# Performance work log

Measured on AMD Instinct MI355X. Metric: run time of the kernel, lower is better.

Reference implementation:

```python
import jax, jax.numpy as jnp
import numpy as np

N_NODES = 1024  # cities (fully connected graph)
N_HID = 128     # config.N: edge-MLP hidden dim (W2: N_HID x 3)
M = 128         # config.M: embedding dim
T = 4           # config.T: message-passing iterations
TAU = 10.0      # config.tau: softmax temperature


def setup_inputs() -> dict:
    key = jax.random.key(0)
    ks = jax.random.split(key, 18)
    u = lambda k, s: jax.random.uniform(k, s, dtype=jnp.float32)
    return dict(
        D=u(ks[0], (N_NODES, N_NODES)),       # pairwise distances graph[v][u]
        dd=u(ks[1], (N_NODES,)),              # graph[depot][v]
        dr=u(ks[2], (N_NODES,)),              # distance_from_robot()
        ddep=u(ks[3], (N_NODES,)),            # distance_from_depot()
        mu0_A1=u(ks[4], (N_NODES, M)),
        mu0_A2=u(ks[5], (N_NODES, M)),
        mu0_B=u(ks[6], (N_NODES, M)),
        W1=u(ks[7], (1, N_HID)),
        W2=u(ks[8], (N_HID, 3)),
        W3_A1=u(ks[9], (M, M + 1)),
        W3_A2=u(ks[10], (M, M + 1)),
        W4_A1=u(ks[11], (M, 1)),
        W4_A2=u(ks[12], (M, 1)),
        W3_B=u(ks[13], (M, M)),
        W4_B=u(ks[14], (M, 2 * M)),
        W5=u(ks[15], (1, M)),
        W6=u(ks[16], (1, M)),
        W7=u(ks[17], (1, M)),
    )


def _edge_scores(D, dd, W1, W2):
    # G[v,u] = W1 @ relu(W2 @ [D[v,u], dd[v], dd[u]])  -> scalar per pair
    h = (D[:, :, None] * W2[:, 0]
         + dd[:, None, None] * W2[:, 1]
         + dd[None, :, None] * W2[:, 2])            # (n, n, N_HID)
    return jnp.maximum(h, 0.0) @ W1[0]              # (n, n)


def _attn(G):
    # p[u,v] = softmax over sources u != v of G[u,v]/tau
    n = G.shape[0]
    Gm = jnp.where(jnp.eye(n, dtype=bool), -jnp.inf, G / TAU)
    return jax.nn.softmax(Gm, axis=0)


def _layer_A(P, wd, mu, Wg, W3, W4, dist):
    # l_v = [ sum_u p_uv * D[u,v] * relu(Wg @ mu_v) ; sum_u p_uv * mu_u ]
    # mu_v <- relu(W3 @ l_v + W4 * dist_v)
    for _ in range(T):
        s = jnp.maximum(mu @ Wg[0], 0.0)                        # (n,)
        l = jnp.concatenate([(wd * s)[:, None], P.T @ mu], 1)   # (n, M+1)
        mu = jnp.maximum(l @ W3.T + dist[:, None] * W4[:, 0][None, :], 0.0)
    return mu


def reference(D, dd, dr, ddep, mu0_A1, mu0_A2, mu0_B,
              W1, W2, W3_A1, W3_A2, W4_A1, W4_A2, W3_B, W4_B, W5, W6, W7):
    # A1 and B use distances / 1000 for edge scores; A2 uses raw distances.
    G_scaled = _edge_scores(D / 1000.0, dd / 1000.0, W1, W2)
    G_raw = _edge_scores(D, dd, W1, W2)
    P1 = _attn(G_scaled)
    P2 = _attn(G_raw)
    wd1 = jnp.sum(P1 * D, axis=0)   # attention-weighted raw edge distance, per v
    wd2 = jnp.sum(P2 * D, axis=0)

    A1 = _layer_A(P1, wd1, mu0_A1, W5, W3_A1, W4_A1, dr)
    A2 = _layer_A(P2, wd2, mu0_A2, W6, W3_A2, W4_A2, ddep)

    bias = jnp.concatenate([A1, A2], axis=1) @ W4_B.T  # (n, M), constant over t
    mu = mu0_B
    for _ in range(T):
        mu = jnp.maximum((P1.T @ mu) @ W3_B.T + bias, 0.0)

    return jnp.maximum(W7 @ jnp.sum(mu, axis=0)[:, None], 0.0)  # (1, 1)
```

## Files before the change

### kernel.cpp

```cpp
#include <hip/hip_runtime.h>
#include <math.h>

#define N 1024
#define M 128

__global__ __launch_bounds__(256) void k_prep(const float* __restrict__ D, float* __restrict__ DT,
    const float* __restrict__ W3A1, const float* __restrict__ W3A2,
    const float* __restrict__ W3B, const float* __restrict__ W4B,
    float* __restrict__ oA1, float* __restrict__ oA2,
    float* __restrict__ oB, float* __restrict__ o4B,
    float* __restrict__ gsum, unsigned int* __restrict__ gcnt) {
  int bx = blockIdx.x, t = threadIdx.x;
  if (bx < 1024) {
    __shared__ float tile[32 * 33];
    int tx = t & 31, ty = t >> 5;
    int bxx = (bx & 31) * 32, by = (bx >> 5) * 32;
#pragma unroll
    for (int i = 0; i < 4; i++)
      tile[(ty + i * 8) * 33 + tx] = D[(size_t)(by + ty + i * 8) * N + bxx + tx];
    __syncthreads();
#pragma unroll
    for (int i = 0; i < 4; i++)
      DT[(size_t)(bxx + ty + i * 8) * N + by + tx] = tile[tx * 33 + ty + i * 8];
  } else if (bx < 1345) {
    int idx = (bx - 1024) * 256 + t;
    const float* in = nullptr; float* op = nullptr; int cols = 0, o = 0;
    if (idx < 16512)      { in = W3A1; op = oA1; cols = 129; o = idx; }
    else if (idx < 33024) { in = W3A2; op = oA2; cols = 129; o = idx - 16512; }
    else if (idx < 49408) { in = W3B;  op = oB;  cols = 128; o = idx - 33024; }
    else if (idx < 82176) { in = W4B;  op = o4B; cols = 256; o = idx - 49408; }
    if (in) { int r = o & 127, c = o >> 7; op[o] = in[r * cols + c]; }
  } else {
    if (t == 0) { *gsum = 0.f; *gcnt = 0u; }
  }
}

__device__ __forceinline__ float blk_max(float v, float* red, int t) {
#pragma unroll
  for (int o = 32; o; o >>= 1) v = fmaxf(v, __shfl_xor(v, o));
  __syncthreads();
  if ((t & 63) == 0) red[t >> 6] = v;
  __syncthreads();
  return fmaxf(fmaxf(red[0], red[1]), fmaxf(red[2], red[3]));
}
__device__ __forceinline__ float blk_sum(float v, float* red, int t) {
#pragma unroll
  for (int o = 32; o; o >>= 1) v += __shfl_xor(v, o);
  __syncthreads();
  if ((t & 63) == 0) red[t >> 6] = v;
  __syncthreads();
  return red[0] + red[1] + red[2] + red[3];
}

__global__ __launch_bounds__(256) void k_edge(const float* __restrict__ DT,
                                              const float* __restrict__ dd,
                                              const float* __restrict__ W1,
                                              const float* __restrict__ W2,
                                              float* __restrict__ PT1, float* __restrict__ PT2,
                                              float* __restrict__ wd1, float* __restrict__ wd2) {
  __shared__ float4 wp[128];
  __shared__ float red[4];
  int t = threadIdx.x, v = blockIdx.x;
  if (t < 128) {
    float4 p;
    p.x = W2[t * 3 + 0]; p.y = W2[t * 3 + 1]; p.z = W2[t * 3 + 2]; p.w = W1[t];
    wp[t] = p;
  }
  __syncthreads();
  float yv = dd[v];
  float x[4], z[4], g[4] = {0.f, 0.f, 0.f, 0.f};
#pragma unroll
  for (int i = 0; i < 4; i++) {
    int u = t + i * 256;
    x[i] = DT[(size_t)v * N + u];
    z[i] = dd[u];
  }
#pragma unroll 2
  for (int k = 0; k < 128; k++) {
    float4 wk = wp[k];
    float cv = yv * wk.z;
#pragma unroll
    for (int i = 0; i < 4; i++) {
      float h = fmaf(x[i], wk.x, fmaf(z[i], wk.y, cv));
      g[i] = fmaf(fmaxf(h, 0.f), wk.w, g[i]);
    }
  }
#pragma unroll
  for (int i = 0; i < 4; i++)
    if (t + i * 256 == v) g[i] = -INFINITY;
  float m = fmaxf(fmaxf(g[0], g[1]), fmaxf(g[2], g[3]));
  m = blk_max(m, red, t);
  float er[4], es[4], sr = 0.f, ss = 0.f;
#pragma unroll
  for (int i = 0; i < 4; i++) {
    er[i] = expf((g[i] - m) * 0.1f);
    es[i] = expf((g[i] - m) * 1e-4f);
    sr += er[i]; ss += es[i];
  }
  sr = blk_sum(sr, red, t);
  ss = blk_sum(ss, red, t);
  float ir = 1.f / sr, is = 1.f / ss;
  float a1 = 0.f, a2 = 0.f;
#pragma unroll
  for (int i = 0; i < 4; i++) {
    int u = t + i * 256;
    float pr = er[i] * ir, ps = es[i] * is;
    PT2[(size_t)v * N + u] = pr;
    PT1[(size_t)v * N + u] = ps;
    a1 += ps * x[i];
    a2 += pr * x[i];
  }
  a1 = blk_sum(a1, red, t);
  a2 = blk_sum(a2, red, t);
  if (t == 0) { wd1[v] = a1; wd2[v] = a2; }
}

__device__ __forceinline__ void gemm4(const float* __restrict__ PT,
                                      const float* __restrict__ cur,
                                      float* __restrict__ As, float* __restrict__ CsP,
                                      int r0, int t) {
#pragma unroll
  for (int i = 0; i < 4; i++) {
    int idx = t + i * 256;
    int row = idx >> 8, c4 = idx & 255;
    ((float4*)As)[row * 256 + c4] = *((const float4*)(PT + (size_t)(r0 + row) * N) + c4);
  }
  __syncthreads();
  const int kc = t >> 5;
  const int cg = t & 31;
  const int u0 = kc * 128;
  float4 acc0 = {0,0,0,0}, acc1 = {0,0,0,0}, acc2 = {0,0,0,0}, acc3 = {0,0,0,0};
  const float* mub = cur + (size_t)u0 * M + cg * 4;
  const float* a0p = As + u0;
  const float* a1p = As + 1024 + u0;
  const float* a2p = As + 2048 + u0;
  const float* a3p = As + 3072 + u0;
#pragma unroll 2
  for (int uu = 0; uu < 128; uu += 4) {
    float4 a0 = *(const float4*)&a0p[uu];
    float4 a1 = *(const float4*)&a1p[uu];
    float4 a2 = *(const float4*)&a2p[uu];
    float4 a3 = *(const float4*)&a3p[uu];
    float4 b0 = *(const float4*)&mub[(size_t)(uu + 0) * M];
    float4 b1 = *(const float4*)&mub[(size_t)(uu + 1) * M];
    float4 b2 = *(const float4*)&mub[(size_t)(uu + 2) * M];
    float4 b3 = *(const float4*)&mub[(size_t)(uu + 3) * M];
#define FMA4(ACC, AV) \
    ACC.x = fmaf(AV.x, b0.x, ACC.x); ACC.y = fmaf(AV.x, b0.y, ACC.y); \
    ACC.z = fmaf(AV.x, b0.z, ACC.z); ACC.w = fmaf(AV.x, b0.w, ACC.w); \
    ACC.x = fmaf(AV.y, b1.x, ACC.x); ACC.y = fmaf(AV.y, b1.y, ACC.y); \
    ACC.z = fmaf(AV.y, b1.z, ACC.z); ACC.w = fmaf(AV.y, b1.w, ACC.w); \
    ACC.x = fmaf(AV.z, b2.x, ACC.x); ACC.y = fmaf(AV.z, b2.y, ACC.y); \
    ACC.z = fmaf(AV.z, b2.z, ACC.z); ACC.w = fmaf(AV.z, b2.w, ACC.w); \
    ACC.x = fmaf(AV.w, b3.x, ACC.x); ACC.y = fmaf(AV.w, b3.y, ACC.y); \
    ACC.z = fmaf(AV.w, b3.z, ACC.z); ACC.w = fmaf(AV.w, b3.w, ACC.w);
    FMA4(acc0, a0) FMA4(acc1, a1) FMA4(acc2, a2) FMA4(acc3, a3)
#undef FMA4
  }
  float* cp = CsP + kc * 512 + cg * 4;
  *(float4*)&cp[0]   = acc0;
  *(float4*)&cp[128] = acc1;
  *(float4*)&cp[256] = acc2;
  *(float4*)&cp[384] = acc3;
  __syncthreads();
#pragma unroll
  for (int i = 0; i < 2; i++) {
    int j = t + i * 256;
    float s = 0.f;
#pragma unroll
    for (int s8 = 0; s8 < 8; s8++) s += CsP[s8 * 512 + j];
    As[j] = s;
  }
}

__global__ __launch_bounds__(256) void k_iterA(
    const float* __restrict__ PT1, const float* __restrict__ PT2,
    const float* __restrict__ cur1, const float* __restrict__ cur2,
    float* __restrict__ nxt1, float* __restrict__ nxt2,
    const float* __restrict__ wd1, const float* __restrict__ wd2,
    const float* __restrict__ dr, const float* __restrict__ ddep,
    const float* __restrict__ W3A1T, const float* __restrict__ W3A2T,
    const float* __restrict__ W4A1, const float* __restrict__ W4A2,
    const float* __restrict__ W5, const float* __restrict__ W6) {
  __shared__ float smem[4096 + 4096 + 4];
  float* As = smem;
  float* CsP = smem + 4096;
  float* swd = smem + 8192;
  int z = blockIdx.z;
  const float* PT = z ? PT2 : PT1;
  const float* cur = z ? cur2 : cur1;
  float* nxt = z ? nxt2 : nxt1;
  const float* wdv = z ? wd2 : wd1;
  const float* dist = z ? ddep : dr;
  const float* W3T = z ? W3A2T : W3A1T;
  const float* W4c = z ? W4A2 : W4A1;
  const float* Wg = z ? W6 : W5;
  int t = threadIdx.x, r0 = blockIdx.x * 4;

  gemm4(PT, cur, As, CsP, r0, t);
  {
    int row = t >> 6, l = t & 63;
    const float* mo = cur + (size_t)(r0 + row) * M;
    float sp = fmaf(mo[l], Wg[l], mo[l + 64] * Wg[l + 64]);
#pragma unroll
    for (int o = 32; o; o >>= 1) sp += __shfl_xor(sp, o);
    if (l == 0) swd[row] = wdv[r0 + row] * fmaxf(sp, 0.f);
  }
  __syncthreads();
  float* Cred = As;

  int col = t & 127, ra = t >> 7;
  float accA = 0.f, accB = 0.f;
  const float* wcol = W3T + 128 + col;
#pragma unroll 4
  for (int m = 0; m < 128; m += 4) {
    float4 c0 = *(const float4*)&Cred[ra * 128 + m];
    float4 c1 = *(const float4*)&Cred[(ra + 2) * 128 + m];
    float w0 = wcol[(m + 0) * 128], w1 = wcol[(m + 1) * 128];
    float w2 = wcol[(m + 2) * 128], w3 = wcol[(m + 3) * 128];
    accA = fmaf(c0.x, w0, fmaf(c0.y, w1, fmaf(c0.z, w2, fmaf(c0.w, w3, accA))));
    accB = fmaf(c1.x, w0, fmaf(c1.y, w1, fmaf(c1.z, w2, fmaf(c1.w, w3, accB))));
  }
  float w30 = W3T[col], w4 = W4c[col];
  float o0 = fmaxf(fmaf(swd[ra], w30, fmaf(dist[r0 + ra], w4, accA)), 0.f);
  float o1 = fmaxf(fmaf(swd[ra + 2], w30, fmaf(dist[r0 + ra + 2], w4, accB)), 0.f);
  nxt[(size_t)(r0 + ra) * M + col] = o0;
  nxt[(size_t)(r0 + ra + 2) * M + col] = o1;
}

__global__ __launch_bounds__(256) void k_iterB(
    const float* __restrict__ PT1, const float* __restrict__ cur, float* __restrict__ nxt,
    const float* __restrict__ W3BT, const float* __restrict__ W4BT, float* __restrict__ biasb,
    const float* __restrict__ A1f, const float* __restrict__ A2f,
    const float* __restrict__ W7, float* __restrict__ gsum, unsigned int* __restrict__ gcnt,
    float* __restrict__ out, int flags) {
  __shared__ float smem[4096 + 4096 + 4];
  float* As = smem;
  float* CsP = smem + 4096;
  float* red = smem + 8192;
  int t = threadIdx.x, r0 = blockIdx.x * 4;

  gemm4(PT1, cur, As, CsP, r0, t);
  __syncthreads();
  float* Cred = As;

  int col = t & 127, ra = t >> 7;
  float bv0, bv1;
  if (flags & 1) {
    bv0 = 0.f; bv1 = 0.f;
    const float* a1a = A1f + (size_t)(r0 + ra) * M;
    const float* a1b = A1f + (size_t)(r0 + ra + 2) * M;
#pragma unroll 4
    for (int c = 0; c < 128; c++) {
      float wv = W4BT[c * 128 + col];
      bv0 = fmaf(a1a[c], wv, bv0);
      bv1 = fmaf(a1b[c], wv, bv1);
    }
    const float* a2a = A2f + (size_t)(r0 + ra) * M;
    const float* a2b = A2f + (size_t)(r0 + ra + 2) * M;
#pragma unroll 4
    for (int c = 0; c < 128; c++) {
      float wv = W4BT[(c + 128) * 128 + col];
      bv0 = fmaf(a2a[c], wv, bv0);
      bv1 = fmaf(a2b[c], wv, bv1);
    }
    biasb[(size_t)(r0 + ra) * M + col] = bv0;
    biasb[(size_t)(r0 + ra + 2) * M + col] = bv1;
  } else {
    bv0 = biasb[(size_t)(r0 + ra) * M + col];
    bv1 = biasb[(size_t)(r0 + ra + 2) * M + col];
  }

  float accA = 0.f, accB = 0.f;
  const float* wcol = W3BT + col;
#pragma unroll 4
  for (int m = 0; m < 128; m += 4) {
    float4 c0 = *(const float4*)&Cred[ra * 128 + m];
    float4 c1 = *(const float4*)&Cred[(ra + 2) * 128 + m];
    float w0 = wcol[(m + 0) * 128], w1 = wcol[(m + 1) * 128];
    float w2 = wcol[(m + 2) * 128], w3 = wcol[(m + 3) * 128];
    accA = fmaf(c0.x, w0, fmaf(c0.y, w1, fmaf(c0.z, w2, fmaf(c0.w, w3, accA))));
    accB = fmaf(c1.x, w0, fmaf(c1.y, w1, fmaf(c1.z, w2, fmaf(c1.w, w3, accB))));
  }
  float o0 = fmaxf(accA + bv0, 0.f);
  float o1 = fmaxf(accB + bv1, 0.f);

  if (!(flags & 2)) {
    nxt[(size_t)(r0 + ra) * M + col] = o0;
    nxt[(size_t)(r0 + ra + 2) * M + col] = o1;
  } else {
    float s = (o0 + o1) * W7[col];
#pragma unroll
    for (int off = 32; off; off >>= 1) s += __shfl_xor(s, off);
    __syncthreads();
    if ((t & 63) == 0) red[t >> 6] = s;
    __syncthreads();
    if (t == 0) {
      float bs = red[0] + red[1] + red[2] + red[3];
      atomicAdd(gsum, bs);
      __threadfence();
      unsigned int old = atomicAdd(gcnt, 1u);
      if (old == 255u) {
        float tot = atomicAdd(gsum, 0.f);
        out[0] = fmaxf(tot, 0.f);
      }
    }
  }
}

extern "C" void kernel_launch(void* const* d_in, const int* in_sizes, int n_in,
                              void* d_out, int out_size, void* d_ws, size_t ws_size,
                              hipStream_t stream) {
  (void)in_sizes; (void)n_in; (void)out_size; (void)ws_size;
  const float* D     = (const float*)d_in[0];
  const float* dd    = (const float*)d_in[1];
  const float* dr    = (const float*)d_in[2];
  const float* ddep  = (const float*)d_in[3];
  const float* mu0A1 = (const float*)d_in[4];
  const float* mu0A2 = (const float*)d_in[5];
  const float* mu0B  = (const float*)d_in[6];
  const float* W1    = (const float*)d_in[7];
  const float* W2    = (const float*)d_in[8];
  const float* W3A1  = (const float*)d_in[9];
  const float* W3A2  = (const float*)d_in[10];
  const float* W4A1  = (const float*)d_in[11];
  const float* W4A2  = (const float*)d_in[12];
  const float* W3B   = (const float*)d_in[13];
  const float* W4B   = (const float*)d_in[14];
  const float* W5    = (const float*)d_in[15];
  const float* W6    = (const float*)d_in[16];
  const float* W7    = (const float*)d_in[17];

  float* w = (float*)d_ws;
  size_t o = 0;
  auto alloc = [&](size_t n) { float* p = w + o; o += n; return p; };
  float* DT    = alloc((size_t)N * N);
  float* PT1   = alloc((size_t)N * N);
  float* PT2   = alloc((size_t)N * N);
  float* wd1   = alloc(N);
  float* wd2   = alloc(N);
  float* W3A1T = alloc(129 * 128);
  float* W3A2T = alloc(129 * 128);
  float* W3BT  = alloc(128 * 128);
  float* W4BT  = alloc(256 * 128);
  float* muA1a = alloc((size_t)N * M); float* muA1b = alloc((size_t)N * M);
  float* muA2a = alloc((size_t)N * M); float* muA2b = alloc((size_t)N * M);
  float* muBa  = alloc((size_t)N * M); float* muBb  = alloc((size_t)N * M);
  float* biasb = alloc((size_t)N * M);
  float* gsum  = alloc(1);
  unsigned int* gcnt = (unsigned int*)alloc(1);

  k_prep<<<1346, 256, 0, stream>>>(D, DT, W3A1, W3A2, W3B, W4B,
                                   W3A1T, W3A2T, W3BT, W4BT, gsum, gcnt);
  k_edge<<<N, 256, 0, stream>>>(DT, dd, W1, W2, PT1, PT2, wd1, wd2);

  const float* c1 = mu0A1;
  const float* c2 = mu0A2;
  float* b1[2] = {muA1a, muA1b};
  float* b2[2] = {muA2a, muA2b};
  for (int it = 0; it < 4; it++) {
    k_iterA<<<dim3(256, 1, 2), 256, 0, stream>>>(PT1, PT2, c1, c2,
        b1[it & 1], b2[it & 1], wd1, wd2, dr, ddep,
        W3A1T, W3A2T, W4A1, W4A2, W5, W6);
    c1 = b1[it & 1];
    c2 = b2[it & 1];
  }

  const float* cB = mu0B;
  float* bB[2] = {muBa, muBb};
  for (int it = 0; it < 4; it++) {
    int flags = (it == 0 ? 1 : 0) | (it == 3 ? 2 : 0);
    k_iterB<<<256, 256, 0, stream>>>(PT1, cB, bB[it & 1],
        W3BT, W4BT, biasb, muA1b, muA2b,
        W7, gsum, gcnt, (float*)d_out, flags);
    cB = bB[it & 1];
  }
}
```

Baseline: 158.6 us.

## Switch propagation GEMMs to bf16 MFMA with transposed bf16 embeddings

Attention matrices, embeddings and W3 weights are now stored in bf16, and the embeddings are kept transposed. Both the P^T@mu and the W3 GEMMs in the A and B iteration kernels run on 16x16x32 bf16 MFMA instructions. Each block now handles 16 rows instead of 4, and the relu(mu@Wg) scalar is computed ahead of time in prep and in the previous iteration's epilogue. This cuts memory traffic for the 1024x1024 attention matrices and moves the FMA work onto matrix cores. In exchange, precision drops to bf16 and grids shrink to 64 or 128 blocks, which may leave many CUs idle.

```diff
diff --git a/kernel.cpp b/kernel.cpp
--- a/kernel.cpp
+++ b/kernel.cpp
@@ -4,11 +4,28 @@
 #define N 1024
 #define M 128
 
-__global__ __launch_bounds__(256) void k_prep(const float* __restrict__ D, float* __restrict__ DT,
+typedef unsigned short us16;
+typedef __attribute__((ext_vector_type(8))) short bf8v;
+typedef __attribute__((ext_vector_type(4))) float f4v;
+
+__device__ __forceinline__ us16 f2bf(float f) {
+  unsigned int u = __float_as_uint(f);
+  unsigned int r = u + 0x7FFFu + ((u >> 16) & 1u);
+  return (us16)(r >> 16);
+}
+
+__global__ __launch_bounds__(256) void k_prep(
+    const float* __restrict__ D, float* __restrict__ DT,
     const float* __restrict__ W3A1, const float* __restrict__ W3A2,
     const float* __restrict__ W3B, const float* __restrict__ W4B,
-    float* __restrict__ oA1, float* __restrict__ oA2,
-    float* __restrict__ oB, float* __restrict__ o4B,
+    float* __restrict__ W4BT,
+    us16* __restrict__ W3A1bf, us16* __restrict__ W3A2bf, us16* __restrict__ W3Bbf,
+    float* __restrict__ w30A1, float* __restrict__ w30A2,
+    const float* __restrict__ mu0A1, const float* __restrict__ mu0A2,
+    const float* __restrict__ mu0B,
+    const float* __restrict__ W5, const float* __restrict__ W6,
+    float* __restrict__ s1, float* __restrict__ s2,
+    us16* __restrict__ muA1T0, us16* __restrict__ muA2T0, us16* __restrict__ muBT0,
     float* __restrict__ gsum, unsigned int* __restrict__ gcnt) {
   int bx = blockIdx.x, t = threadIdx.x;
   if (bx < 1024) {
@@ -22,14 +39,54 @@
 #pragma unroll
     for (int i = 0; i < 4; i++)
       DT[(size_t)(bxx + ty + i * 8) * N + by + tx] = tile[tx * 33 + ty + i * 8];
+  } else if (bx < 1152) {
+    int idx = (bx - 1024) * 256 + t;
+    int r = idx & 127, c = idx >> 7;
+    W4BT[idx] = W4B[r * 256 + c];
+  } else if (bx < 1344) {
+    int idx = (bx - 1152) * 256 + t;
+    int mat = idx >> 14, o = idx & 16383;
+    int c = o >> 7, m = o & 127;
+    if (mat == 0)      W3A1bf[o] = f2bf(W3A1[c * 129 + m + 1]);
+    else if (mat == 1) W3A2bf[o] = f2bf(W3A2[c * 129 + m + 1]);
+    else               W3Bbf[o]  = f2bf(W3B[c * 128 + m]);
   } else if (bx < 1345) {
-    int idx = (bx - 1024) * 256 + t;
-    const float* in = nullptr; float* op = nullptr; int cols = 0, o = 0;
-    if (idx < 16512)      { in = W3A1; op = oA1; cols = 129; o = idx; }
-    else if (idx < 33024) { in = W3A2; op = oA2; cols = 129; o = idx - 16512; }
-    else if (idx < 49408) { in = W3B;  op = oB;  cols = 128; o = idx - 33024; }
-    else if (idx < 82176) { in = W4B;  op = o4B; cols = 256; o = idx - 49408; }
-    if (in) { int r = o & 127, c = o >> 7; op[o] = in[r * cols + c]; }
+    if (t < 128) w30A1[t] = W3A1[t * 129];
+    else if (t < 256) w30A2[t - 128] = W3A2[(t - 128) * 129];
+  } else if (bx < 1473) {
+    int idx = (bx - 1345) * 256 + t;
+    int row = idx >> 4, l16 = idx & 15;
+    int chain = row >> 10, r = row & 1023;
+    const float* mu0 = chain ? mu0A2 : mu0A1;
+    const float* Wg = chain ? W6 : W5;
+    float* sb = chain ? s2 : s1;
+    const float* mp = mu0 + (size_t)r * M + l16 * 8;
+    float4 a0 = *(const float4*)mp, a1 = *(const float4*)(mp + 4);
+    float4 g0 = *(const float4*)(Wg + l16 * 8), g1 = *(const float4*)(Wg + l16 * 8 + 4);
+    float sp = a0.x * g0.x + a0.y * g0.y + a0.z * g0.z + a0.w * g0.w
+             + a1.x * g1.x + a1.y * g1.y + a1.z * g1.z + a1.w * g1.w;
+#pragma unroll
+    for (int o = 8; o; o >>= 1) sp += __shfl_xor(sp, o);
+    if (l16 == 0) sb[r] = sp;
+  } else if (bx < 1857) {
+    int rel = bx - 1473;
+    int mat = rel >> 7, tile = rel & 127;
+    int u0 = (tile >> 2) * 32, c0 = (tile & 3) * 32;
+    const float* src = mat == 0 ? mu0A1 : (mat == 1 ? mu0A2 : mu0B);
+    us16* dst = mat == 0 ? muA1T0 : (mat == 1 ? muA2T0 : muBT0);
+    __shared__ float tl[32 * 33];
+    int tx = t & 31, ty = t >> 5;
+#pragma unroll
+    for (int i = 0; i < 4; i++)
+      tl[(ty + i * 8) * 33 + tx] = src[(size_t)(u0 + ty + i * 8) * M + c0 + tx];
+    __syncthreads();
+    int c = t >> 3, uq = (t & 7) * 4;
+    ushort4 p;
+    p.x = f2bf(tl[(uq + 0) * 33 + c]);
+    p.y = f2bf(tl[(uq + 1) * 33 + c]);
+    p.z = f2bf(tl[(uq + 2) * 33 + c]);
+    p.w = f2bf(tl[(uq + 3) * 33 + c]);
+    *(ushort4*)(dst + (size_t)(c0 + c) * N + u0 + uq) = p;
   } else {
     if (t == 0) { *gsum = 0.f; *gcnt = 0u; }
   }
@@ -56,7 +113,7 @@
                                               const float* __restrict__ dd,
                                               const float* __restrict__ W1,
                                               const float* __restrict__ W2,
-                                              float* __restrict__ PT1, float* __restrict__ PT2,
+                                              us16* __restrict__ PT1bf, us16* __restrict__ PT2bf,
                                               float* __restrict__ wd1, float* __restrict__ wd2) {
   __shared__ float4 wp[128];
   __shared__ float red[4];
@@ -68,13 +125,11 @@
   }
   __syncthreads();
   float yv = dd[v];
-  float x[4], z[4], g[4] = {0.f, 0.f, 0.f, 0.f};
-#pragma unroll
-  for (int i = 0; i < 4; i++) {
-    int u = t + i * 256;
-    x[i] = DT[(size_t)v * N + u];
-    z[i] = dd[u];
-  }
+  float4 xv = *(const float4*)&DT[(size_t)v * N + t * 4];
+  float4 zv = *(const float4*)&dd[t * 4];
+  float x[4] = {xv.x, xv.y, xv.z, xv.w};
+  float z[4] = {zv.x, zv.y, zv.z, zv.w};
+  float g[4] = {0.f, 0.f, 0.f, 0.f};
 #pragma unroll 2
   for (int k = 0; k < 128; k++) {
     float4 wk = wp[k];
@@ -87,7 +142,7 @@
   }
 #pragma unroll
   for (int i = 0; i < 4; i++)
-    if (t + i * 256 == v) g[i] = -INFINITY;
+    if (t * 4 + i == v) g[i] = -INFINITY;
   float m = fmaxf(fmaxf(g[0], g[1]), fmaxf(g[2], g[3]));
   m = blk_max(m, red, t);
   float er[4], es[4], sr = 0.f, ss = 0.f;
@@ -101,206 +156,222 @@
   ss = blk_sum(ss, red, t);
   float ir = 1.f / sr, is = 1.f / ss;
   float a1 = 0.f, a2 = 0.f;
-#pragma unroll
-  for (int i = 0; i < 4; i++) {
-    int u = t + i * 256;
-    float pr = er[i] * ir, ps = es[i] * is;
-    PT2[(size_t)v * N + u] = pr;
-    PT1[(size_t)v * N + u] = ps;
-    a1 += ps * x[i];
-    a2 += pr * x[i];
-  }
+  ushort4 p1, p2;
+  float ps0 = es[0] * is, ps1 = es[1] * is, ps2 = es[2] * is, ps3 = es[3] * is;
+  float pr0 = er[0] * ir, pr1 = er[1] * ir, pr2 = er[2] * ir, pr3 = er[3] * ir;
+  p1.x = f2bf(ps0); p1.y = f2bf(ps1); p1.z = f2bf(ps2); p1.w = f2bf(ps3);
+  p2.x = f2bf(pr0); p2.y = f2bf(pr1); p2.z = f2bf(pr2); p2.w = f2bf(pr3);
+  *(ushort4*)(PT1bf + (size_t)v * N + t * 4) = p1;
+  *(ushort4*)(PT2bf + (size_t)v * N + t * 4) = p2;
+  a1 = ps0 * x[0] + ps1 * x[1] + ps2 * x[2] + ps3 * x[3];
+  a2 = pr0 * x[0] + pr1 * x[1] + pr2 * x[2] + pr3 * x[3];
   a1 = blk_sum(a1, red, t);
   a2 = blk_sum(a2, red, t);
   if (t == 0) { wd1[v] = a1; wd2[v] = a2; }
 }
 
-__device__ __forceinline__ void gemm4(const float* __restrict__ PT,
-                                      const float* __restrict__ cur,
-                                      float* __restrict__ As, float* __restrict__ CsP,
-                                      int r0, int t) {
-#pragma unroll
-  for (int i = 0; i < 4; i++) {
-    int idx = t + i * 256;
-    int row = idx >> 8, c4 = idx & 255;
-    ((float4*)As)[row * 256 + c4] = *((const float4*)(PT + (size_t)(r0 + row) * N) + c4);
-  }
-  __syncthreads();
-  const int kc = t >> 5;
-  const int cg = t & 31;
-  const int u0 = kc * 128;
-  float4 acc0 = {0,0,0,0}, acc1 = {0,0,0,0}, acc2 = {0,0,0,0}, acc3 = {0,0,0,0};
-  const float* mub = cur + (size_t)u0 * M + cg * 4;
-  const float* a0p = As + u0;
-  const float* a1p = As + 1024 + u0;
-  const float* a2p = As + 2048 + u0;
-  const float* a3p = As + 3072 + u0;
-#pragma unroll 2
-  for (int uu = 0; uu < 128; uu += 4) {
-    float4 a0 = *(const float4*)&a0p[uu];
-    float4 a1 = *(const float4*)&a1p[uu];
-    float4 a2 = *(const float4*)&a2p[uu];
-    float4 a3 = *(const float4*)&a3p[uu];
-    float4 b0 = *(const float4*)&mub[(size_t)(uu + 0) * M];
-    float4 b1 = *(const float4*)&mub[(size_t)(uu + 1) * M];
-    float4 b2 = *(const float4*)&mub[(size_t)(uu + 2) * M];
-    float4 b3 = *(const float4*)&mub[(size_t)(uu + 3) * M];
-#define FMA4(ACC, AV) \
-    ACC.x = fmaf(AV.x, b0.x, ACC.x); ACC.y = fmaf(AV.x, b0.y, ACC.y); \
-    ACC.z = fmaf(AV.x, b0.z, ACC.z); ACC.w = fmaf(AV.x, b0.w, ACC.w); \
-    ACC.x = fmaf(AV.y, b1.x, ACC.x); ACC.y = fmaf(AV.y, b1.y, ACC.y); \
-    ACC.z = fmaf(AV.y, b1.z, ACC.z); ACC.w = fmaf(AV.y, b1.w, ACC.w); \
-    ACC.x = fmaf(AV.z, b2.x, ACC.x); ACC.y = fmaf(AV.z, b2.y, ACC.y); \
-    ACC.z = fmaf(AV.z, b2.z, ACC.z); ACC.w = fmaf(AV.z, b2.w, ACC.w); \
-    ACC.x = fmaf(AV.w, b3.x, ACC.x); ACC.y = fmaf(AV.w, b3.y, ACC.y); \
-    ACC.z = fmaf(AV.w, b3.z, ACC.z); ACC.w = fmaf(AV.w, b3.w, ACC.w);
-    FMA4(acc0, a0) FMA4(acc1, a1) FMA4(acc2, a2) FMA4(acc3, a3)
-#undef FMA4
-  }
-  float* cp = CsP + kc * 512 + cg * 4;
-  *(float4*)&cp[0]   = acc0;
-  *(float4*)&cp[128] = acc1;
-  *(float4*)&cp[256] = acc2;
-  *(float4*)&cp[384] = acc3;
-  __syncthreads();
-#pragma unroll
-  for (int i = 0; i < 2; i++) {
-    int j = t + i * 256;
-    float s = 0.f;
-#pragma unroll
-    for (int s8 = 0; s8 < 8; s8++) s += CsP[s8 * 512 + j];
-    As[j] = s;
+#define CS_LD 140
+
+__device__ __forceinline__ void mfma_gemm16(const us16* __restrict__ PT,
+                                            const us16* __restrict__ curT,
+                                            float* __restrict__ Cs,
+                                            int r0, int t) {
+  const int l = t & 63, w = t >> 6;
+  const int g = l >> 4, c16 = l & 15;
+  const int col0 = w * 32;
+  f4v acc0 = {0.f, 0.f, 0.f, 0.f}, acc1 = {0.f, 0.f, 0.f, 0.f};
+  const bf8v* ap  = (const bf8v*)(PT + (size_t)(r0 + c16) * N + g * 8);
+  const bf8v* bp0 = (const bf8v*)(curT + (size_t)(col0 + c16) * N + g * 8);
+  const bf8v* bp1 = (const bf8v*)(curT + (size_t)(col0 + 16 + c16) * N + g * 8);
+#pragma unroll 4
+  for (int kk = 0; kk < 32; kk++) {
+    bf8v a = ap[kk * 4];
+    bf8v b0 = bp0[kk * 4];
+    bf8v b1 = bp1[kk * 4];
+    acc0 = __builtin_amdgcn_mfma_f32_16x16x32_bf16(a, b0, acc0, 0, 0, 0);
+    acc1 = __builtin_amdgcn_mfma_f32_16x16x32_bf16(a, b1, acc1, 0, 0, 0);
+  }
+#pragma unroll
+  for (int reg = 0; reg < 4; reg++) {
+    Cs[(g * 4 + reg) * CS_LD + col0 + c16] = acc0[reg];
+    Cs[(g * 4 + reg) * CS_LD + col0 + 16 + c16] = acc1[reg];
+  }
+  __syncthreads();
+}
+
+__device__ __forceinline__ void mfma_epi(const float* __restrict__ Cs,
+                                         const us16* __restrict__ W3bf,
+                                         int t, f4v& o0, f4v& o1) {
+  const int l = t & 63, w = t >> 6;
+  const int g = l >> 4, c16 = l & 15;
+  const int col0 = w * 32;
+  o0 = (f4v){0.f, 0.f, 0.f, 0.f};
+  o1 = (f4v){0.f, 0.f, 0.f, 0.f};
+  const bf8v* w3p0 = (const bf8v*)(W3bf + (size_t)(col0 + c16) * M + g * 8);
+  const bf8v* w3p1 = (const bf8v*)(W3bf + (size_t)(col0 + 16 + c16) * M + g * 8);
+#pragma unroll
+  for (int m0 = 0; m0 < 4; m0++) {
+    const float* cr = &Cs[c16 * CS_LD + m0 * 32 + g * 8];
+    float4 ca = *(const float4*)cr;
+    float4 cb = *(const float4*)(cr + 4);
+    bf8v a2;
+    a2[0] = (short)f2bf(ca.x); a2[1] = (short)f2bf(ca.y);
+    a2[2] = (short)f2bf(ca.z); a2[3] = (short)f2bf(ca.w);
+    a2[4] = (short)f2bf(cb.x); a2[5] = (short)f2bf(cb.y);
+    a2[6] = (short)f2bf(cb.z); a2[7] = (short)f2bf(cb.w);
+    bf8v b0 = w3p0[m0 * 4];
+    bf8v b1 = w3p1[m0 * 4];
+    o0 = __builtin_amdgcn_mfma_f32_16x16x32_bf16(a2, b0, o0, 0, 0, 0);
+    o1 = __builtin_amdgcn_mfma_f32_16x16x32_bf16(a2, b1, o1, 0, 0, 0);
   }
 }
 
 __global__ __launch_bounds__(256) void k_iterA(
-    const float* __restrict__ PT1, const float* __restrict__ PT2,
-    const float* __restrict__ cur1, const float* __restrict__ cur2,
-    float* __restrict__ nxt1, float* __restrict__ nxt2,
+    const us16* __restrict__ PT1bf, const us16* __restrict__ PT2bf,
+    const us16* __restrict__ curT1, const us16* __restrict__ curT2,
+    us16* __restrict__ nxtT1, us16* __restrict__ nxtT2,
+    float* __restrict__ muf1, float* __restrict__ muf2, int writef,
+    float* __restrict__ s1buf, float* __restrict__ s2buf,
     const float* __restrict__ wd1, const float* __restrict__ wd2,
     const float* __restrict__ dr, const float* __restrict__ ddep,
-    const float* __restrict__ W3A1T, const float* __restrict__ W3A2T,
+    const us16* __restrict__ W3A1bf, const us16* __restrict__ W3A2bf,
+    const float* __restrict__ w30A1, const float* __restrict__ w30A2,
     const float* __restrict__ W4A1, const float* __restrict__ W4A2,
     const float* __restrict__ W5, const float* __restrict__ W6) {
-  __shared__ float smem[4096 + 4096 + 4];
-  float* As = smem;
-  float* CsP = smem + 4096;
-  float* swd = smem + 8192;
-  int z = blockIdx.z;
-  const float* PT = z ? PT2 : PT1;
-  const float* cur = z ? cur2 : cur1;
-  float* nxt = z ? nxt2 : nxt1;
+  __shared__ float Cs[16 * CS_LD];
+  const int z = blockIdx.z;
+  const us16* PT = z ? PT2bf : PT1bf;
+  const us16* curT = z ? curT2 : curT1;
+  us16* nxtT = z ? nxtT2 : nxtT1;
+  float* muf = z ? muf2 : muf1;
+  float* sbuf = z ? s2buf : s1buf;
   const float* wdv = z ? wd2 : wd1;
   const float* dist = z ? ddep : dr;
-  const float* W3T = z ? W3A2T : W3A1T;
+  const us16* W3bf = z ? W3A2bf : W3A1bf;
+  const float* w30 = z ? w30A2 : w30A1;
   const float* W4c = z ? W4A2 : W4A1;
   const float* Wg = z ? W6 : W5;
-  int t = threadIdx.x, r0 = blockIdx.x * 4;
-
-  gemm4(PT, cur, As, CsP, r0, t);
+  const int t = threadIdx.x, r0 = blockIdx.x * 16;
+  const int l = t & 63, w = t >> 6;
+  const int g = l >> 4, c16 = l & 15;
+  const int col0 = w * 32;
+
+  mfma_gemm16(PT, curT, Cs, r0, t);
+  f4v o0, o1;
+  mfma_epi(Cs, W3bf, t, o0, o1);
+
+  float w30a = w30[col0 + c16], w30b = w30[col0 + 16 + c16];
+  float w4a = W4c[col0 + c16], w4b = W4c[col0 + 16 + c16];
+  float ov0[4], ov1[4];
+  ushort4 pk0, pk1;
+#pragma unroll
+  for (int reg = 0; reg < 4; reg++) {
+    int r = r0 + g * 4 + reg;
+    float sv = wdv[r] * fmaxf(sbuf[r], 0.f);
+    float dv = dist[r];
+    ov0[reg] = fmaxf(o0[reg] + sv * w30a + dv * w4a, 0.f);
+    ov1[reg] = fmaxf(o1[reg] + sv * w30b + dv * w4b, 0.f);
+  }
+  pk0.x = f2bf(ov0[0]); pk0.y = f2bf(ov0[1]); pk0.z = f2bf(ov0[2]); pk0.w = f2bf(ov0[3]);
+  pk1.x = f2bf(ov1[0]); pk1.y = f2bf(ov1[1]); pk1.z = f2bf(ov1[2]); pk1.w = f2bf(ov1[3]);
+  *(ushort4*)(nxtT + (size_t)(col0 + c16) * N + r0 + g * 4) = pk0;
+  *(ushort4*)(nxtT + (size_t)(col0 + 16 + c16) * N + r0 + g * 4) = pk1;
+
+  __syncthreads();
+#pragma unroll
+  for (int reg = 0; reg < 4; reg++) {
+    Cs[(g * 4 + reg) * CS_LD + col0 + c16] = ov0[reg];
+    Cs[(g * 4 + reg) * CS_LD + col0 + 16 + c16] = ov1[reg];
+  }
+  __syncthreads();
   {
-    int row = t >> 6, l = t & 63;
-    const float* mo = cur + (size_t)(r0 + row) * M;
-    float sp = fmaf(mo[l], Wg[l], mo[l + 64] * Wg[l + 64]);
-#pragma unroll
-    for (int o = 32; o; o >>= 1) sp += __shfl_xor(sp, o);
-    if (l == 0) swd[row] = wdv[r0 + row] * fmaxf(sp, 0.f);
-  }
-  __syncthreads();
-  float* Cred = As;
-
-  int col = t & 127, ra = t >> 7;
-  float accA = 0.f, accB = 0.f;
-  const float* wcol = W3T + 128 + col;
-#pragma unroll 4
-  for (int m = 0; m < 128; m += 4) {
-    float4 c0 = *(const float4*)&Cred[ra * 128 + m];
-    float4 c1 = *(const float4*)&Cred[(ra + 2) * 128 + m];
-    float w0 = wcol[(m + 0) * 128], w1 = wcol[(m + 1) * 128];
-    float w2 = wcol[(m + 2) * 128], w3 = wcol[(m + 3) * 128];
-    accA = fmaf(c0.x, w0, fmaf(c0.y, w1, fmaf(c0.z, w2, fmaf(c0.w, w3, accA))));
-    accB = fmaf(c1.x, w0, fmaf(c1.y, w1, fmaf(c1.z, w2, fmaf(c1.w, w3, accB))));
-  }
-  float w30 = W3T[col], w4 = W4c[col];
-  float o0 = fmaxf(fmaf(swd[ra], w30, fmaf(dist[r0 + ra], w4, accA)), 0.f);
-  float o1 = fmaxf(fmaf(swd[ra + 2], w30, fmaf(dist[r0 + ra + 2], w4, accB)), 0.f);
-  nxt[(size_t)(r0 + ra) * M + col] = o0;
-  nxt[(size_t)(r0 + ra + 2) * M + col] = o1;
+    int row = t >> 4, l16 = t & 15;
+    const float* cr = &Cs[row * CS_LD + l16 * 8];
+    float4 x0 = *(const float4*)cr, x1 = *(const float4*)(cr + 4);
+    float4 g0 = *(const float4*)(Wg + l16 * 8), g1 = *(const float4*)(Wg + l16 * 8 + 4);
+    float sp = x0.x * g0.x + x0.y * g0.y + x0.z * g0.z + x0.w * g0.w
+             + x1.x * g1.x + x1.y * g1.y + x1.z * g1.z + x1.w * g1.w;
+#pragma unroll
+    for (int o = 8; o; o >>= 1) sp += __shfl_xor(sp, o);
+    if (l16 == 0) sbuf[r0 + row] = sp;
+  }
+  if (writef) {
+#pragma unroll
+    for (int i = 0; i < 8; i++) {
+      int e = t + i * 256;
+      int r = e >> 7, c = e & 127;
+      muf[(size_t)(r0 + r) * M + c] = Cs[r * CS_LD + c];
+    }
+  }
 }
 
 __global__ __launch_bounds__(256) void k_iterB(
-    const float* __restrict__ PT1, const float* __restrict__ cur, float* __restrict__ nxt,
-    const float* __restrict__ W3BT, const float* __restrict__ W4BT, float* __restrict__ biasb,
-    const float* __restrict__ A1f, const float* __restrict__ A2f,
-    const float* __restrict__ W7, float* __restrict__ gsum, unsigned int* __restrict__ gcnt,
-    float* __restrict__ out, int flags) {
-  __shared__ float smem[4096 + 4096 + 4];
-  float* As = smem;
-  float* CsP = smem + 4096;
-  float* red = smem + 8192;
-  int t = threadIdx.x, r0 = blockIdx.x * 4;
-
-  gemm4(PT1, cur, As, CsP, r0, t);
-  __syncthreads();
-  float* Cred = As;
-
-  int col = t & 127, ra = t >> 7;
-  float bv0, bv1;
+    const us16* __restrict__ PT1bf, const us16* __restrict__ curT, us16* __restrict__ nxtT,
+    const us16* __restrict__ W3Bbf, const float* __restrict__ W4BT,
+    float* __restrict__ biasb,
+    const float* __restrict__ muf1, const float* __restrict__ muf2,
+    const float* __restrict__ W7, float* __restrict__ gsum,
+    unsigned int* __restrict__ gcnt, float* __restrict__ out, int flags) {
+  __shared__ float Cs[16 * CS_LD];
+  __shared__ float redf[4];
+  const int t = threadIdx.x, r0 = blockIdx.x * 16;
+  const int l = t & 63, w = t >> 6;
+  const int g = l >> 4, c16 = l & 15;
+  const int col0 = w * 32;
+
   if (flags & 1) {
-    bv0 = 0.f; bv1 = 0.f;
-    const float* a1a = A1f + (size_t)(r0 + ra) * M;
-    const float* a1b = A1f + (size_t)(r0 + ra + 2) * M;
-#pragma unroll 4
+    int col = t & 127, rh = (t >> 7) * 8;
+    float bacc[8] = {0, 0, 0, 0, 0, 0, 0, 0};
+#pragma unroll 2
     for (int c = 0; c < 128; c++) {
-      float wv = W4BT[c * 128 + col];
-      bv0 = fmaf(a1a[c], wv, bv0);
-      bv1 = fmaf(a1b[c], wv, bv1);
+      float wA = W4BT[c * 128 + col];
+      float wB = W4BT[(c + 128) * 128 + col];
+#pragma unroll
+      for (int j = 0; j < 8; j++) {
+        bacc[j] = fmaf(muf1[(size_t)(r0 + rh + j) * M + c], wA, bacc[j]);
+        bacc[j] = fmaf(muf2[(size_t)(r0 + rh + j) * M + c], wB, bacc[j]);
+      }
     }
-    const float* a2a = A2f + (size_t)(r0 + ra) * M;
-    const float* a2b = A2f + (size_t)(r0 + ra + 2) * M;
-#pragma unroll 4
-    for (int c = 0; c < 128; c++) {
-      float wv = W4BT[(c + 128) * 128 + col];
-      bv0 = fmaf(a2a[c], wv, bv0);
-      bv1 = fmaf(a2b[c], wv, bv1);
-    }
-    biasb[(size_t)(r0 + ra) * M + col] = bv0;
-    biasb[(size_t)(r0 + ra + 2) * M + col] = bv1;
+#pragma unroll
+    for (int j = 0; j < 8; j++)
+      biasb[(size_t)(r0 + rh + j) * M + col] = bacc[j];
+    __syncthreads();
+  }
+
+  mfma_gemm16(PT1bf, curT, Cs, r0, t);
+  f4v o0, o1;
+  mfma_epi(Cs, W3Bbf, t, o0, o1);
+
+  float ov0[4], ov1[4];
+#pragma unroll
+  for (int reg = 0; reg < 4; reg++) {
+    int r = r0 + g * 4 + reg;
+    ov0[reg] = fmaxf(o0[reg] + biasb[(size_t)r * M + col0 + c16], 0.f);
+    ov1[reg] = fmaxf(o1[reg] + biasb[(size_t)r * M + col0 + 16 + c16], 0.f);
+  }
+
+  if (!(flags & 2)) {
+    ushort4 pk0, pk1;
+    pk0.x = f2bf(ov0[0]); pk0.y = f2bf(ov0[1]); pk0.z = f2bf(ov0[2]); pk0.w = f2bf(ov0[3]);
+    pk1.x = f2bf(ov1[0]); pk1.y = f2bf(ov1[1]); pk1.z = f2bf(ov1[2]); pk1.w = f2bf(ov1[3]);
+    *(ushort4*)(nxtT + (size_t)(col0 + c16) * N + r0 + g * 4) = pk0;
+    *(ushort4*)(nxtT + (size_t)(col0 + 16 + c16) * N + r0 + g * 4) = pk1;
   } else {
-    bv0 = biasb[(size_t)(r0 + ra) * M + col];
-    bv1 = biasb[(size_t)(r0 + ra + 2) * M + col];
-  }
-
-  float accA = 0.f, accB = 0.f;
-  const float* wcol = W3BT + col;
-#pragma unroll 4
-  for (int m = 0; m < 128; m += 4) {
-    float4 c0 = *(const float4*)&Cred[ra * 128 + m];
-    float4 c1 = *(const float4*)&Cred[(ra + 2) * 128 + m];
-    float w0 = wcol[(m + 0) * 128], w1 = wcol[(m + 1) * 128];
-    float w2 = wcol[(m + 2) * 128], w3 = wcol[(m + 3) * 128];
-    accA = fmaf(c0.x, w0, fmaf(c0.y, w1, fmaf(c0.z, w2, fmaf(c0.w, w3, accA))));
-    accB = fmaf(c1.x, w0, fmaf(c1.y, w1, fmaf(c1.z, w2, fmaf(c1.w, w3, accB))));
-  }
-  float o0 = fmaxf(accA + bv0, 0.f);
-  float o1 = fmaxf(accB + bv1, 0.f);
-
-  if (!(flags & 2)) {
-    nxt[(size_t)(r0 + ra) * M + col] = o0;
-    nxt[(size_t)(r0 + ra + 2) * M + col] = o1;
-  } else {
-    float s = (o0 + o1) * W7[col];
-#pragma unroll
-    for (int off = 32; off; off >>= 1) s += __shfl_xor(s, off);
-    __syncthreads();
-    if ((t & 63) == 0) red[t >> 6] = s;
+    float w7a = W7[col0 + c16], w7b = W7[col0 + 16 + c16];
+    float part = 0.f;
+#pragma unroll
+    for (int reg = 0; reg < 4; reg++)
+      part += ov0[reg] * w7a + ov1[reg] * w7b;
+#pragma unroll
+    for (int o = 32; o; o >>= 1) part += __shfl_xor(part, o);
+    if (l == 0) redf[w] = part;
     __syncthreads();
     if (t == 0) {
-      float bs = red[0] + red[1] + red[2] + red[3];
+      float bs = redf[0] + redf[1] + redf[2] + redf[3];
       atomicAdd(gsum, bs);
       __threadfence();
       unsigned int old = atomicAdd(gcnt, 1u);
-      if (old == 255u) {
+      if (old == 63u) {
         float tot = atomicAdd(gsum, 0.f);
         out[0] = fmaxf(tot, 0.f);
       }
@@ -331,47 +402,62 @@
   const float* W6    = (const float*)d_in[16];
   const float* W7    = (const float*)d_in[17];
 
-  float* w = (float*)d_ws;
+  float* wsf = (float*)d_ws;
   size_t o = 0;
-  auto alloc = [&](size_t n) { float* p = w + o; o += n; return p; };
-  float* DT    = alloc((size_t)N * N);
-  float* PT1   = alloc((size_t)N * N);
-  float* PT2   = alloc((size_t)N * N);
-  float* wd1   = alloc(N);
-  float* wd2   = alloc(N);
-  float* W3A1T = alloc(129 * 128);
-  float* W3A2T = alloc(129 * 128);
-  float* W3BT  = alloc(128 * 128);
-  float* W4BT  = alloc(256 * 128);
-  float* muA1a = alloc((size_t)N * M); float* muA1b = alloc((size_t)N * M);
-  float* muA2a = alloc((size_t)N * M); float* muA2b = alloc((size_t)N * M);
-  float* muBa  = alloc((size_t)N * M); float* muBb  = alloc((size_t)N * M);
-  float* biasb = alloc((size_t)N * M);
-  float* gsum  = alloc(1);
+  auto alloc = [&](size_t n) { float* p = wsf + o; o += n; return p; };
+  float* DT     = alloc((size_t)N * N);
+  us16* PT1bf   = (us16*)alloc((size_t)N * N / 2);
+  us16* PT2bf   = (us16*)alloc((size_t)N * N / 2);
+  float* W4BT   = alloc(256 * 128);
+  us16* W3A1bf  = (us16*)alloc(128 * 128 / 2);
+  us16* W3A2bf  = (us16*)alloc(128 * 128 / 2);
+  us16* W3Bbf   = (us16*)alloc(128 * 128 / 2);
+  float* w30A1  = alloc(128);
+  float* w30A2  = alloc(128);
+  float* s1     = alloc(N);
+  float* s2     = alloc(N);
+  float* wd1    = alloc(N);
+  float* wd2    = alloc(N);
+  us16* muA1T0  = (us16*)alloc((size_t)M * N / 2);
+  us16* muA2T0  = (us16*)alloc((size_t)M * N / 2);
+  us16* muBT0   = (us16*)alloc((size_t)M * N / 2);
+  us16* muA1Ta  = (us16*)alloc((size_t)M * N / 2);
+  us16* muA1Tb  = (us16*)alloc((size_t)M * N / 2);
+  us16* muA2Ta  = (us16*)alloc((size_t)M * N / 2);
+  us16* muA2Tb  = (us16*)alloc((size_t)M * N / 2);
+  us16* muBTa   = (us16*)alloc((size_t)M * N / 2);
+  us16* muBTb   = (us16*)alloc((size_t)M * N / 2);
+  float* muf1   = alloc((size_t)N * M);
+  float* muf2   = alloc((size_t)N * M);
+  float* biasb  = alloc((size_t)N * M);
+  float* gsum   = alloc(1);
   unsigned int* gcnt = (unsigned int*)alloc(1);
 
-  k_prep<<<1346, 256, 0, stream>>>(D, DT, W3A1, W3A2, W3B, W4B,
-                                   W3A1T, W3A2T, W3BT, W4BT, gsum, gcnt);
-  k_edge<<<N, 256, 0, stream>>>(DT, dd, W1, W2, PT1, PT2, wd1, wd2);
-
-  const float* c1 = mu0A1;
-  const float* c2 = mu0A2;
-  float* b1[2] = {muA1a, muA1b};
-  float* b2[2] = {muA2a, muA2b};
+  k_prep<<<1858, 256, 0, stream>>>(D, DT, W3A1, W3A2, W3B, W4B, W4BT,
+                                   W3A1bf, W3A2bf, W3Bbf, w30A1, w30A2,
+                                   mu0A1, mu0A2, mu0B, W5, W6, s1, s2,
+                                   muA1T0, muA2T0, muBT0, gsum, gcnt);
+  k_edge<<<N, 256, 0, stream>>>(DT, dd, W1, W2, PT1bf, PT2bf, wd1, wd2);
+
+  const us16* c1 = muA1T0;
+  const us16* c2 = muA2T0;
+  us16* b1[2] = {muA1Ta, muA1Tb};
+  us16* b2[2] = {muA2Ta, muA2Tb};
   for (int it = 0; it < 4; it++) {
-    k_iterA<<<dim3(256, 1, 2), 256, 0, stream>>>(PT1, PT2, c1, c2,
-        b1[it & 1], b2[it & 1], wd1, wd2, dr, ddep,
-        W3A1T, W3A2T, W4A1, W4A2, W5, W6);
+    k_iterA<<<dim3(64, 1, 2), 256, 0, stream>>>(PT1bf, PT2bf, c1, c2,
+        b1[it & 1], b2[it & 1], muf1, muf2, (it == 3) ? 1 : 0,
+        s1, s2, wd1, wd2, dr, ddep,
+        W3A1bf, W3A2bf, w30A1, w30A2, W4A1, W4A2, W5, W6);
     c1 = b1[it & 1];
     c2 = b2[it & 1];
   }
 
-  const float* cB = mu0B;
-  float* bB[2] = {muBa, muBb};
+  const us16* cB = muBT0;
+  us16* bB[2] = {muBTa, muBTb};
   for (int it = 0; it < 4; it++) {
     int flags = (it == 0 ? 1 : 0) | (it == 3 ? 2 : 0);
-    k_iterB<<<256, 256, 0, stream>>>(PT1, cB, bB[it & 1],
-        W3BT, W4BT, biasb, muA1b, muA2b,
+    k_iterB<<<64, 256, 0, stream>>>(PT1bf, cB, bB[it & 1],
+        W3Bbf, W4BT, biasb, muf1, muf2,
         W7, gsum, gcnt, (float*)d_out, flags);
     cB = bB[it & 1];
   }
```

New measurement: 195.2 us. +23.1%, slower.
